# Optimization experiments

Hardware: AMD Instinct MI355X
Metric: run time of the kernel (lower is better)

Reference implementation:

```python
import jax, jax.numpy as jnp
import numpy as np

N = 256            # state_space_size
BF = (4, 4, 4)     # branching_factors
T = 128            # time steps
D_IN = 64          # input_size
D_T = 64           # time_embedding_size
BATCH = 16
NUM_NODES = N * 4 * 4 * 4  # 16384


def setup_inputs() -> dict:
    key = jax.random.key(0)
    ks = jax.random.split(key, 20)

    def lin_w(k, out_d, in_d):
        return jax.random.normal(k, (out_d, in_d), jnp.float32) / np.sqrt(in_d)

    inp = {
        "x": jax.random.normal(ks[0], (BATCH, T, N), jnp.float32),
        "t_embeddings_schedule": jax.random.normal(ks[1], (T, D_T), jnp.float32),
        "input_vector": jax.random.normal(ks[2], (BATCH, T, D_IN), jnp.float32),
        # Fanout node params
        "Wa": lin_w(ks[3], NUM_NODES, N),
        "ba": jnp.zeros((NUM_NODES,), jnp.float32),
        "Wt": lin_w(ks[4], NUM_NODES, D_T),
        "Wi": lin_w(ks[5], NUM_NODES, D_IN),
        # Node with bf[:3]=[4,4,4]: reduces last 4 -> [N,4,4]
        "w3": jax.random.normal(ks[6], (N, 4, 4, 4), jnp.float32) * np.sqrt(2.0 / (4 + N * 16)),
        "tW3": lin_w(ks[7], N * 16, D_T),
        "tb3": jnp.zeros((N * 16,), jnp.float32),
        # Node with bf[:2]=[4,4]
        "w2": jax.random.normal(ks[8], (N, 4, 4), jnp.float32) * np.sqrt(2.0 / (4 + N * 4)),
        "tW2": lin_w(ks[9], N * 4, D_T),
        "tb2": jnp.zeros((N * 4,), jnp.float32),
        # Node with bf[:1]=[4]
        "w1": jax.random.normal(ks[10], (N, 4), jnp.float32) * np.sqrt(2.0 / (4 + N)),
        "tW1": lin_w(ks[11], N, D_T),
        "tb1": jnp.zeros((N,), jnp.float32),
    }
    return inp


def _node(act, t_emb, w, tW, tb):
    # act: [..., T, N, *bf]; w: [N, *bf]; reduce last branching dim
    tproj = (t_emb @ tW.T + tb).reshape(t_emb.shape[0], *w.shape[:-1])  # [T, N, *bf[:-1]]
    pre = (w * act).sum(-1) + tproj  # broadcast over leading batch dims
    return jax.nn.softplus(pre)


def reference(x, t_embeddings_schedule, input_vector, Wa, ba, Wt, Wi,
              w3, tW3, tb3, w2, tW2, tb2, w1, tW1, tb1):
    t_emb = t_embeddings_schedule
    # Fanout: [B, T, N] -> [B, T, N, 4, 4, 4]
    pre = x @ Wa.T + ba + (t_emb @ Wt.T) + input_vector @ Wi.T  # [B, T, NUM_NODES]
    act = jax.nn.softplus(pre.reshape(*pre.shape[:-1], N, *BF))
    # Tree: deepest node first (insert-at-1 order in original)
    act = _node(act, t_emb, w3, tW3, tb3)  # [B, T, N, 4, 4]
    act = _node(act, t_emb, w2, tW2, tb2)  # [B, T, N, 4]
    act = _node(act, t_emb, w1, tW1, tb1)  # [B, T, N]
    return act
```

## Files before the change

kernel.cpp:

```cpp
#include <hip/hip_runtime.h>

typedef __attribute__((ext_vector_type(4))) float f32x4;
typedef __attribute__((ext_vector_type(8))) __bf16 bf16x8;
typedef __attribute__((ext_vector_type(8))) unsigned short u16x8;

__device__ __forceinline__ unsigned short f2bf(float f) {
    unsigned int u = __float_as_uint(f);
    u += 0x7fffu + ((u >> 16) & 1u);
    return (unsigned short)(u >> 16);
}

__device__ __forceinline__ float softplus_f(float x) {
    float e = __expf(-fabsf(x));
    return fmaxf(x, 0.0f) + __logf(1.0f + e);
}

typedef __attribute__((address_space(3))) void lds_void_t;
typedef __attribute__((address_space(1))) void glb_void_t;

__device__ __forceinline__ void load16_to_lds(const void* g, const void* l) {
    __builtin_amdgcn_global_load_lds((glb_void_t*)(unsigned long long)g,
                                     (lds_void_t*)(unsigned int)(unsigned long long)l,
                                     16, 0, 0);
}

#define REPACK_NB 4
#define REPACK_BLOCKS 864
__global__ __launch_bounds__(256) void repack(
        const float* __restrict__ x, const float* __restrict__ iv,
        const float* __restrict__ temb,
        const float* __restrict__ Wa, const float* __restrict__ Wi,
        const float* __restrict__ Wt,
        unsigned short* __restrict__ Abf ) {
    const int stride = REPACK_BLOCKS * 256;
    const int tid0 = blockIdx.x * 256 + threadIdx.x;
    float4 f[REPACK_NB][2];
    #pragma unroll
    for (int c = 0; c < REPACK_NB; ++c) {
        const int idx = tid0 + c * stride;
        const bool isA = idx < 98304;
        const int widx = isA ? idx : idx - 98304;
        const int row = widx / 48;
        const int kk  = (widx % 48) * 8;
        const float* p0 = isA ? (x    + (size_t)row * 256) : (Wa + (size_t)row * 256);
        const float* p1 = isA ? (iv   + (size_t)row * 64)  : (Wi + (size_t)row * 64);
        const float* p2 = isA ? (temb + (size_t)(row & 127) * 64) : (Wt + (size_t)row * 64);
        const float* src = (kk < 256) ? (p0 + kk) : ((kk < 320) ? (p1 + kk - 256) : (p2 + kk - 320));
        f[c][0] = ((const float4*)src)[0];
        f[c][1] = ((const float4*)src)[1];
    }
    #pragma unroll
    for (int c = 0; c < REPACK_NB; ++c) {
        const int idx = tid0 + c * stride;
        u16x8 o;
        o[0] = f2bf(f[c][0].x); o[1] = f2bf(f[c][0].y); o[2] = f2bf(f[c][0].z); o[3] = f2bf(f[c][0].w);
        o[4] = f2bf(f[c][1].x); o[5] = f2bf(f[c][1].y); o[6] = f2bf(f[c][1].z); o[7] = f2bf(f[c][1].w);
        *(u16x8*)(Abf + (size_t)idx * 8) = o;
    }
}

__global__ __launch_bounds__(256) void tproj(
        const float* __restrict__ temb,
        const float* __restrict__ tW3, const float* __restrict__ tb3,
        const float* __restrict__ tW2, const float* __restrict__ tb2,
        const float* __restrict__ tW1, const float* __restrict__ tb1,
        float* __restrict__ tp3T, float* __restrict__ tp2T, float* __restrict__ tp1T) {
    __shared__ float se[32 * 64];
    const int tid = threadIdx.x;
    const int tbase = blockIdx.y * 32;
    for (int i = tid; i < 32 * 64; i += 256) se[i] = temb[tbase * 64 + i];
    __syncthreads();
    const int j = blockIdx.x * 64 + (tid >> 2);
    const float* W; const float* bias; float* outp; int jl;
    if      (j < 4096) { W = tW3; bias = tb3; outp = tp3T; jl = j; }
    else if (j < 5120) { W = tW2; bias = tb2; outp = tp2T; jl = j - 4096; }
    else               { W = tW1; bias = tb1; outp = tp1T; jl = j - 5120; }
    float4 wreg[16];
    const float4* wrow = (const float4*)(W + (size_t)jl * 64);
    #pragma unroll
    for (int k = 0; k < 16; ++k) wreg[k] = wrow[k];
    const float b = bias[jl];
    #pragma unroll
    for (int s = 0; s < 8; ++s) {
        const int tl = (tid & 3) + s * 4;
        const float4* e4 = (const float4*)&se[tl * 64];
        float a = b;
        #pragma unroll
        for (int k = 0; k < 16; ++k) {
            float4 e = e4[k];
            a += wreg[k].x * e.x + wreg[k].y * e.y + wreg[k].z * e.z + wreg[k].w * e.w;
        }
        outp[(size_t)jl * 128 + tbase + tl] = a;
    }
}

__global__ __launch_bounds__(256, 4)
void fused_gemm_tree(const unsigned short* __restrict__ Wbf,
                     const unsigned short* __restrict__ Abf,
                     const float* __restrict__ ba,
                     const float* __restrict__ tp3T, const float* __restrict__ tp2T,
                     const float* __restrict__ tp1T,
                     const float* __restrict__ w3, const float* __restrict__ w2,
                     const float* __restrict__ w1,
                     float* __restrict__ out) {
    __shared__ unsigned short sW[128 * 32];
    __shared__ unsigned short sA[128 * 32];

    const int tid  = threadIdx.x;
    const int wave = tid >> 6;
    const int lane = tid & 63;
    const int wr = wave >> 1;
    const int wc = wave & 1;
    const int lane15 = lane & 15;
    const int quad = lane >> 4;

    const int node0 = blockIdx.x * 128;
    const int m0    = blockIdx.y * 128;

    f32x4 acc[4][4];
    const f32x4 zero = {0.0f, 0.0f, 0.0f, 0.0f};
    #pragma unroll
    for (int i = 0; i < 4; ++i)
        #pragma unroll
        for (int j = 0; j < 4; ++j) acc[i][j] = zero;

    const int wrow = wr * 64 + lane15;
    const int arow = wc * 64 + lane15;
    const int koff = quad * 8;

    const unsigned short* aBase = Wbf + (size_t)node0 * 384;
    const unsigned short* bBase = Abf + (size_t)m0 * 384;

    for (int k0 = 0; k0 < 384; k0 += 32) {
        __syncthreads();
        #pragma unroll
        for (int r = 0; r < 2; ++r) {
            const int chunk = r * 256 + tid;
            const int row   = chunk >> 2;
            const int kk    = k0 + (chunk & 3) * 8;
            load16_to_lds(aBase + (size_t)row * 384 + kk, &sW[(r * 256 + wave * 64) * 8]);
            load16_to_lds(bBase + (size_t)row * 384 + kk, &sA[(r * 256 + wave * 64) * 8]);
        }
        __syncthreads();

        bf16x8 af[4], bfr[4];
        #pragma unroll
        for (int i = 0; i < 4; ++i) af[i]  = *(const bf16x8*)&sW[(wrow + i * 16) * 32 + koff];
        #pragma unroll
        for (int j = 0; j < 4; ++j) bfr[j] = *(const bf16x8*)&sA[(arow + j * 16) * 32 + koff];
        #pragma unroll
        for (int i = 0; i < 4; ++i)
            #pragma unroll
            for (int j = 0; j < 4; ++j)
                acc[i][j] = __builtin_amdgcn_mfma_f32_16x16x32_bf16(af[i], bfr[j], acc[i][j], 0, 0, 0);
    }

    const int n = blockIdx.x * 2 + wr;

    float bav[4][4], w3v[4][4], w2v[4], w1v[4];
    #pragma unroll
    for (int i = 0; i < 4; ++i) {
        #pragma unroll
        for (int r = 0; r < 4; ++r) {
            const int nl = i * 16 + quad * 4 + r;
            bav[i][r] = ba[node0 + wr * 64 + nl];
            w3v[i][r] = w3[n * 64 + nl];
        }
        w2v[i] = w2[n * 16 + i * 4 + quad];
        w1v[i] = w1[n * 4 + i];
    }

    const int tbase = wc * 64 + lane15;
    float s1[4] = {0.0f, 0.0f, 0.0f, 0.0f};

    #pragma unroll
    for (int i = 0; i < 4; ++i) {
        const float* tp3row = tp3T + (size_t)(n * 16 + i * 4 + quad) * 128;
        const float* tp2row = tp2T + (size_t)(n * 4 + i) * 128;
        #pragma unroll
        for (int j = 0; j < 4; ++j) {
            const int t = tbase + j * 16;
            float p3 = 0.0f;
            #pragma unroll
            for (int r = 0; r < 4; ++r) {
                float a0 = softplus_f(acc[i][j][r] + bav[i][r]);
                p3 = fmaf(a0, w3v[i][r], p3);
            }
            float a3 = softplus_f(p3 + tp3row[t]);
            float c2 = a3 * w2v[i];
            c2 += __shfl_xor(c2, 16);
            c2 += __shfl_xor(c2, 32);
            float a2 = softplus_f(c2 + tp2row[t]);
            s1[j] = fmaf(a2, w1v[i], s1[j]);
        }
    }
    #pragma unroll
    for (int j = 0; j < 4; ++j) {
        const int t = tbase + j * 16;
        float o = softplus_f(s1[j] + tp1T[(size_t)n * 128 + t]);
        if (quad == 0) out[(size_t)(m0 + t) * 256 + n] = o;
    }
}

extern "C" void kernel_launch(void* const* d_in, const int* in_sizes, int n_in,
                              void* d_out, int out_size, void* d_ws, size_t ws_size,
                              hipStream_t stream) {
    const float* x    = (const float*)d_in[0];
    const float* temb = (const float*)d_in[1];
    const float* iv   = (const float*)d_in[2];
    const float* Wa   = (const float*)d_in[3];
    const float* ba   = (const float*)d_in[4];
    const float* Wt   = (const float*)d_in[5];
    const float* Wi   = (const float*)d_in[6];
    const float* w3   = (const float*)d_in[7];
    const float* tW3  = (const float*)d_in[8];
    const float* tb3  = (const float*)d_in[9];
    const float* w2   = (const float*)d_in[10];
    const float* tW2  = (const float*)d_in[11];
    const float* tb2  = (const float*)d_in[12];
    const float* w1   = (const float*)d_in[13];
    const float* tW1  = (const float*)d_in[14];
    const float* tb1  = (const float*)d_in[15];
    float* out = (float*)d_out;

    char* ws = (char*)d_ws;
    unsigned short* Abf = (unsigned short*)(ws);
    unsigned short* Wbf = (unsigned short*)(ws + 1572864);
    float* tp3T = (float*)(ws + 14155776);
    float* tp2T = (float*)(ws + 16252928);
    float* tp1T = (float*)(ws + 16777216);

    repack<<<dim3(REPACK_BLOCKS), dim3(256), 0, stream>>>(x, iv, temb, Wa, Wi, Wt, Abf);
    tproj<<<dim3(84, 4), dim3(256), 0, stream>>>(temb, tW3, tb3, tW2, tb2, tW1, tb1,
                                                 tp3T, tp2T, tp1T);
    fused_gemm_tree<<<dim3(128, 16), dim3(256), 0, stream>>>(Wbf, Abf, ba, tp3T, tp2T, tp1T,
                                                             w3, w2, w1, out);
}
```

Baseline: 162.0 us.

## Swizzle LDS tiles, prefetch epilogue params, and spread final stores across quads

Applies an XOR swizzle to the k-chunk position when filling the shared-memory tiles and reads back with the matching swizzle, aiming to cut LDS bank conflicts on the bf16x8 fragment loads. All epilogue parameters (bias, tree weights, time projections) are now loaded into registers before the GEMM loop so their global latency overlaps the main loop. The final softplus and store are spread over the four quads instead of only quad 0 writing. This raises register pressure, which may hurt occupancy.

Result: slower. 196.2 us (+21.1%).

```diff
diff --git a/kernel.cpp b/kernel.cpp
--- a/kernel.cpp
+++ b/kernel.cpp
@@ -116,6 +116,29 @@
 
     const int node0 = blockIdx.x * 128;
     const int m0    = blockIdx.y * 128;
+    const int n     = blockIdx.x * 2 + wr;
+    const int tbase = wc * 64 + lane15;
+
+    float bav[4][4], w3v[4][4], w2v[4], w1v[4], tp3v[4][4], tp2v[4][4], tp1v[4];
+    #pragma unroll
+    for (int i = 0; i < 4; ++i) {
+        const float* tp3row = tp3T + (size_t)(n * 16 + i * 4 + quad) * 128;
+        const float* tp2row = tp2T + (size_t)(n * 4 + i) * 128;
+        #pragma unroll
+        for (int r = 0; r < 4; ++r) {
+            const int nl = i * 16 + quad * 4 + r;
+            bav[i][r] = ba[node0 + wr * 64 + nl];
+            w3v[i][r] = w3[n * 64 + nl];
+        }
+        #pragma unroll
+        for (int j = 0; j < 4; ++j) {
+            tp3v[i][j] = tp3row[tbase + j * 16];
+            tp2v[i][j] = tp2row[tbase + j * 16];
+        }
+        w2v[i] = w2[n * 16 + i * 4 + quad];
+        w1v[i] = w1[n * 4 + i];
+        tp1v[i] = tp1T[(size_t)n * 128 + tbase + i * 16];
+    }
 
     f32x4 acc[4][4];
     const f32x4 zero = {0.0f, 0.0f, 0.0f, 0.0f};
@@ -126,7 +149,7 @@
 
     const int wrow = wr * 64 + lane15;
     const int arow = wc * 64 + lane15;
-    const int koff = quad * 8;
+    const int swz  = lane15 & 3;
 
     const unsigned short* aBase = Wbf + (size_t)node0 * 384;
     const unsigned short* bBase = Abf + (size_t)m0 * 384;
@@ -134,20 +157,22 @@
     for (int k0 = 0; k0 < 384; k0 += 32) {
         __syncthreads();
         #pragma unroll
-        for (int r = 0; r < 2; ++r) {
-            const int chunk = r * 256 + tid;
-            const int row   = chunk >> 2;
-            const int kk    = k0 + (chunk & 3) * 8;
-            load16_to_lds(aBase + (size_t)row * 384 + kk, &sW[(r * 256 + wave * 64) * 8]);
-            load16_to_lds(bBase + (size_t)row * 384 + kk, &sA[(r * 256 + wave * 64) * 8]);
+        for (int rr = 0; rr < 2; ++rr) {
+            const int p = rr * 256 + tid;
+            const int row = p >> 2;
+            const int kchunk = (p & 3) ^ (row & 3);
+            const size_t soff = (size_t)row * 384 + k0 + kchunk * 8;
+            load16_to_lds(aBase + soff, &sW[(size_t)(rr * 256 + wave * 64) * 8]);
+            load16_to_lds(bBase + soff, &sA[(size_t)(rr * 256 + wave * 64) * 8]);
         }
         __syncthreads();
 
+        const int cpos = (quad ^ swz) * 8;
         bf16x8 af[4], bfr[4];
         #pragma unroll
-        for (int i = 0; i < 4; ++i) af[i]  = *(const bf16x8*)&sW[(wrow + i * 16) * 32 + koff];
-        #pragma unroll
-        for (int j = 0; j < 4; ++j) bfr[j] = *(const bf16x8*)&sA[(arow + j * 16) * 32 + koff];
+        for (int i = 0; i < 4; ++i) af[i]  = *(const bf16x8*)&sW[(wrow + i * 16) * 32 + cpos];
+        #pragma unroll
+        for (int j = 0; j < 4; ++j) bfr[j] = *(const bf16x8*)&sA[(arow + j * 16) * 32 + cpos];
         #pragma unroll
         for (int i = 0; i < 4; ++i)
             #pragma unroll
@@ -155,50 +180,37 @@
                 acc[i][j] = __builtin_amdgcn_mfma_f32_16x16x32_bf16(af[i], bfr[j], acc[i][j], 0, 0, 0);
     }
 
-    const int n = blockIdx.x * 2 + wr;
-
-    float bav[4][4], w3v[4][4], w2v[4], w1v[4];
+    float s1[4] = {0.0f, 0.0f, 0.0f, 0.0f};
     #pragma unroll
     for (int i = 0; i < 4; ++i) {
         #pragma unroll
-        for (int r = 0; r < 4; ++r) {
-            const int nl = i * 16 + quad * 4 + r;
-            bav[i][r] = ba[node0 + wr * 64 + nl];
-            w3v[i][r] = w3[n * 64 + nl];
-        }
-        w2v[i] = w2[n * 16 + i * 4 + quad];
-        w1v[i] = w1[n * 4 + i];
-    }
-
-    const int tbase = wc * 64 + lane15;
-    float s1[4] = {0.0f, 0.0f, 0.0f, 0.0f};
-
-    #pragma unroll
-    for (int i = 0; i < 4; ++i) {
-        const float* tp3row = tp3T + (size_t)(n * 16 + i * 4 + quad) * 128;
-        const float* tp2row = tp2T + (size_t)(n * 4 + i) * 128;
-        #pragma unroll
         for (int j = 0; j < 4; ++j) {
-            const int t = tbase + j * 16;
             float p3 = 0.0f;
             #pragma unroll
             for (int r = 0; r < 4; ++r) {
                 float a0 = softplus_f(acc[i][j][r] + bav[i][r]);
                 p3 = fmaf(a0, w3v[i][r], p3);
             }
-            float a3 = softplus_f(p3 + tp3row[t]);
+            float a3 = softplus_f(p3 + tp3v[i][j]);
             float c2 = a3 * w2v[i];
             c2 += __shfl_xor(c2, 16);
             c2 += __shfl_xor(c2, 32);
-            float a2 = softplus_f(c2 + tp2row[t]);
+            float a2 = softplus_f(c2 + tp2v[i][j]);
             s1[j] = fmaf(a2, w1v[i], s1[j]);
         }
     }
-    #pragma unroll
-    for (int j = 0; j < 4; ++j) {
+    {
+        const int j = quad;
+        float sj = s1[0];
+        sj = (j == 1) ? s1[1] : sj;
+        sj = (j == 2) ? s1[2] : sj;
+        sj = (j == 3) ? s1[3] : sj;
+        float tq = tp1v[0];
+        tq = (j == 1) ? tp1v[1] : tq;
+        tq = (j == 2) ? tp1v[2] : tq;
+        tq = (j == 3) ? tp1v[3] : tq;
         const int t = tbase + j * 16;
-        float o = softplus_f(s1[j] + tp1T[(size_t)n * 128 + t]);
-        if (quad == 0) out[(size_t)(m0 + t) * 256 + n] = o;
+        out[(size_t)(m0 + t) * 256 + n] = softplus_f(sj + tq);
     }
 }
 
```
